# Optimization experiments

Hardware: AMD Instinct MI355X
Metric: run time of the kernel (lower is better)

## Reference

```python
import jax, jax.numpy as jnp
import numpy as np

H = 512      # hidden_size
NH = 8       # num_attention_heads
HD = H // NH # attention_head_size
B, S = 2, 4096


def setup_inputs() -> dict:
    key = jax.random.key(0)
    ks = jax.random.split(key, 9)
    sc = 1.0 / np.sqrt(H)
    return {
        "hidden_states": jax.random.normal(ks[0], (B, S, H), dtype=jnp.float32),
        "Wq": jax.random.normal(ks[1], (H, H), dtype=jnp.float32) * sc,
        "bq": jnp.zeros((H,), dtype=jnp.float32),
        "Wk": jax.random.normal(ks[2], (H, H), dtype=jnp.float32) * sc,
        "bk": jnp.zeros((H,), dtype=jnp.float32),
        "Wv": jax.random.normal(ks[3], (H, H), dtype=jnp.float32) * sc,
        "bv": jnp.zeros((H,), dtype=jnp.float32),
        "Wo": jax.random.normal(ks[4], (H, H), dtype=jnp.float32) * sc,
        "bo": jnp.zeros((H,), dtype=jnp.float32),
    }


def reference(hidden_states, Wq, bq, Wk, bk, Wv, bv, Wo, bo):
    # QKV projections (nn.Linear: x @ W.T + b)
    def split_heads(x):  # [B,S,H] -> [B,NH,S,HD]
        return x.reshape(B, S, NH, HD).transpose(0, 2, 1, 3)

    q = split_heads(hidden_states @ Wq.T + bq)
    k = split_heads(hidden_states @ Wk.T + bk)
    v = split_heads(hidden_states @ Wv.T + bv)

    scores = jnp.einsum("bhqd,bhkd->bhqk", q, k) / np.sqrt(HD)
    probs = jax.nn.softmax(scores, axis=-1)  # dropout is identity in eval
    ctx = jnp.einsum("bhqk,bhkd->bhqd", probs, v)
    ctx = ctx.transpose(0, 2, 1, 3).reshape(B, S, H)
    return ctx @ Wo.T + bo
```

## Files before the change

kernel.cpp:

```cpp
#include <hip/hip_runtime.h>
#include <hip/hip_bf16.h>
#include <math.h>


typedef __bf16 bf16;
typedef __bf16 bf16x2v __attribute__((ext_vector_type(2)));
typedef __bf16 bf16x4 __attribute__((ext_vector_type(4)));
typedef __bf16 bf16x8 __attribute__((ext_vector_type(8)));
typedef float  f32x4  __attribute__((ext_vector_type(4)));
typedef unsigned int u32x4 __attribute__((ext_vector_type(4)));

#define MFMA16(a, b, c) __builtin_amdgcn_mfma_f32_16x16x32_bf16((a), (b), (c), 0, 0, 0)

__device__ __forceinline__ void gll16(const bf16* g, bf16* l) {
    __builtin_amdgcn_global_load_lds(
        (const __attribute__((address_space(1))) void*)g,
        (__attribute__((address_space(3))) void*)l, 16, 0, 0);
}

__device__ __forceinline__ unsigned int pack2(float lo, float hi) {
    bf16x2v t = {(bf16)lo, (bf16)hi};
    return __builtin_bit_cast(unsigned int, t);
}

__global__ __launch_bounds__(256) void cvt_f32_bf16(const float* __restrict__ src,
                                                    bf16* __restrict__ dst, int n) {
    int i = (blockIdx.x * 256 + threadIdx.x) * 4;
    if (i >= n) return;
    float4 v = *reinterpret_cast<const float4*>(src + i);
    bf16x4 o = {(bf16)v.x, (bf16)v.y, (bf16)v.z, (bf16)v.w};
    *reinterpret_cast<bf16x4*>(dst + i) = o;
}

__global__ __launch_bounds__(256) void cvt_w4(const float* __restrict__ a,
                                              const float* __restrict__ b,
                                              const float* __restrict__ c,
                                              const float* __restrict__ d,
                                              bf16* __restrict__ out) {
    const int y = blockIdx.y;
    const float* src = (y == 0) ? a : (y == 1) ? b : (y == 2) ? c : d;
    int i = (blockIdx.x * 256 + threadIdx.x) * 4;
    float4 v = *reinterpret_cast<const float4*>(src + i);
    bf16x4 o = {(bf16)v.x, (bf16)v.y, (bf16)v.z, (bf16)v.w};
    *reinterpret_cast<bf16x4*>(out + y * 262144 + i) = o;
}

template <int MODE>
__global__ __launch_bounds__(256) void gemm_bt(const bf16* __restrict__ A,
                                               const bf16* __restrict__ W,
                                               const float* __restrict__ b0,
                                               const float* __restrict__ b1,
                                               const float* __restrict__ b2,
                                               bf16* __restrict__ dstbf,
                                               float* __restrict__ dstf) {
    __shared__ bf16 sA[128 * 64];
    __shared__ bf16 sB[128 * 64];

    const int tid = threadIdx.x;
    const int w   = tid >> 6;
    const int l   = tid & 63;
    const int m0  = blockIdx.y * 128;
    const int n0  = blockIdx.x * 128;
    const int z   = blockIdx.z;

    const bf16*  Wz   = (MODE == 0) ? (W + z * 262144) : W;
    const float* bias = (MODE == 0) ? (z == 0 ? b0 : (z == 1 ? b1 : b2)) : b0;
    const float  scale = (MODE == 0 && z == 0) ? 0.125f * 1.4426950408889634f : 1.0f;

    const int wr = (w >> 1) * 64, wc = (w & 1) * 64;
    const int fr = l & 15, fg = l >> 4;

    const int srow0 = tid >> 3;
    const int sgr   = (tid & 7) ^ (srow0 & 7);
    const int ldso  = srow0 * 64 + (tid & 7) * 8;

    f32x4 acc[4][4];
    const f32x4 zero = {0.f, 0.f, 0.f, 0.f};
#pragma unroll
    for (int i = 0; i < 4; i++)
#pragma unroll
        for (int j = 0; j < 4; j++) acc[i][j] = zero;

    for (int kt = 0; kt < 512; kt += 64) {
        __syncthreads();
#pragma unroll
        for (int p = 0; p < 4; p++) {
            const int row = srow0 + 32 * p;
            gll16(A  + (m0 + row) * 512 + kt + sgr * 8, &sA[p * 2048 + ldso]);
            gll16(Wz + (n0 + row) * 512 + kt + sgr * 8, &sB[p * 2048 + ldso]);
        }
        __syncthreads();

#pragma unroll
        for (int ks = 0; ks < 2; ks++) {
            bf16x8 af[4], bfg[4];
#pragma unroll
            for (int mi = 0; mi < 4; mi++)
                af[mi] = *reinterpret_cast<const bf16x8*>(
                    &sA[(wr + mi * 16 + fr) * 64 + (((4 * ks + fg) ^ (fr & 7)) << 3)]);
#pragma unroll
            for (int ni = 0; ni < 4; ni++)
                bfg[ni] = *reinterpret_cast<const bf16x8*>(
                    &sB[(wc + ni * 16 + fr) * 64 + (((4 * ks + fg) ^ (fr & 7)) << 3)]);
#pragma unroll
            for (int mi = 0; mi < 4; mi++)
#pragma unroll
                for (int ni = 0; ni < 4; ni++)
                    acc[mi][ni] = MFMA16(af[mi], bfg[ni], acc[mi][ni]);
        }
    }

#pragma unroll
    for (int mi = 0; mi < 4; mi++) {
#pragma unroll
        for (int ni = 0; ni < 4; ni++) {
            const int gcol = n0 + wc + ni * 16 + fr;
            const float bc = bias[gcol];
#pragma unroll
            for (int r = 0; r < 4; r++) {
                const int grow = m0 + wr + mi * 16 + fg * 4 + r;
                float v = acc[mi][ni][r] + bc;
                if (MODE == 0) {
                    v *= scale;
                    const int bb = grow >> 12, s = grow & 4095;
                    const int hh = gcol >> 6, dd = gcol & 63;
                    size_t idx;
                    if (z == 2) {
                        idx = (size_t)2 * 4194304 +
                              ((size_t)((bb * 8 + hh) * 64 + dd)) * 4096 + s;
                    } else {
                        idx = (size_t)z * 4194304 +
                              ((size_t)((bb * 8 + hh) * 4096 + s) << 6) + dd;
                    }
                    dstbf[idx] = (bf16)v;
                } else {
                    dstf[grow * 512 + gcol] = v;
                }
            }
        }
    }
}

__global__ __launch_bounds__(256, 2) void attn_kernel(const bf16* __restrict__ Q,
                                                      const bf16* __restrict__ K,
                                                      const bf16* __restrict__ Vt,
                                                      bf16* __restrict__ ctx) {
    __shared__ bf16 sKb[2][4096];
    __shared__ bf16 sVb[2][4096];

    const int tid = threadIdx.x;
    const int w   = tid >> 6;
    const int l   = tid & 63;
    const int fr  = l & 15, fg = l >> 4;

    int n = blockIdx.y * 32 + blockIdx.x;
    n = (n & 7) * 64 + (n >> 3);
    const int bh = n >> 5;
    const int q0 = (n & 31) * 128;
    const size_t base = (size_t)bh * 262144;

    const int srow0 = tid >> 3;
    const int sgr   = (tid & 7) ^ (srow0 & 7);
    const int ldso  = srow0 * 64 + (tid & 7) * 8;

    const int ko0 = fr * 64 + (((0 + fg) ^ (fr & 7)) << 3);
    const int ko1 = fr * 64 + (((4 + fg) ^ (fr & 7)) << 3);

#define STAGE(buf, tt)                                                              \
    do {                                                                            \
        _Pragma("unroll")                                                           \
        for (int p = 0; p < 2; p++) {                                               \
            const int row_ = srow0 + 32 * p;                                        \
            gll16(K  + base + (size_t)((tt) + row_) * 64 + sgr * 8,                 \
                  &sKb[buf][p * 2048 + ldso]);                                      \
            gll16(Vt + base + (size_t)row_ * 4096 + (tt) + sgr * 8,                 \
                  &sVb[buf][p * 2048 + ldso]);                                      \
        }                                                                           \
    } while (0)

    bf16x8 qf[2][2];
#pragma unroll
    for (int qb = 0; qb < 2; qb++)
#pragma unroll
        for (int ks = 0; ks < 2; ks++)
            qf[ks][qb] = *reinterpret_cast<const bf16x8*>(
                Q + base + (size_t)(q0 + 32 * w + 16 * qb + fr) * 64 + ks * 32 + fg * 8);

    const bf16 one = (bf16)1.0f;
    const bf16x8 ones = {one, one, one, one, one, one, one, one};

    const f32x4 zero = {0.f, 0.f, 0.f, 0.f};
    f32x4 o[4][2];
#pragma unroll
    for (int db = 0; db < 4; db++)
#pragma unroll
        for (int qb = 0; qb < 2; qb++) o[db][qb] = zero;
    f32x4 lacc[2] = {zero, zero};

    STAGE(0, 0);

    int pb = 0;
    for (int t = 0; t < 4096; t += 64, pb ^= 1) {
        __syncthreads();
        if (t + 64 < 4096) STAGE(pb ^ 1, t + 64);

        const bf16* kb = sKb[pb];
        const bf16* vb = sVb[pb];

        f32x4 sc[4][2];
        __builtin_amdgcn_s_setprio(1);
#pragma unroll
        for (int kvb = 0; kvb < 4; kvb++) {
            const bf16x8 kf0 = *reinterpret_cast<const bf16x8*>(kb + ko0 + kvb * 1024);
            const bf16x8 kf1 = *reinterpret_cast<const bf16x8*>(kb + ko1 + kvb * 1024);
#pragma unroll
            for (int qb = 0; qb < 2; qb++) {
                sc[kvb][qb] = MFMA16(kf0, qf[0][qb], zero);
                sc[kvb][qb] = MFMA16(kf1, qf[1][qb], sc[kvb][qb]);
            }
        }
        __builtin_amdgcn_s_setprio(0);

        bf16x8 vf[2][4];
#pragma unroll
        for (int db = 0; db < 4; db++) {
            vf[0][db] = *reinterpret_cast<const bf16x8*>(vb + ko0 + db * 1024);
            vf[1][db] = *reinterpret_cast<const bf16x8*>(vb + ko1 + db * 1024);
        }

        bf16x8 pf[2][2];
#pragma unroll
        for (int qb = 0; qb < 2; qb++) {
            unsigned int c[4][2];
#pragma unroll
            for (int kvb = 0; kvb < 4; kvb++) {
                const float p0 = __builtin_amdgcn_exp2f(sc[kvb][qb][0]);
                const float p1 = __builtin_amdgcn_exp2f(sc[kvb][qb][1]);
                const float p2 = __builtin_amdgcn_exp2f(sc[kvb][qb][2]);
                const float p3 = __builtin_amdgcn_exp2f(sc[kvb][qb][3]);
                c[kvb][0] = pack2(p0, p1);
                c[kvb][1] = pack2(p2, p3);
            }
#pragma unroll
            for (int ks = 0; ks < 2; ks++) {
                unsigned int a0 = c[2 * ks][0], b0 = c[2 * ks + 1][0];
                unsigned int a1 = c[2 * ks][1], b1 = c[2 * ks + 1][1];
                asm("v_permlane32_swap_b32 %0, %1" : "+v"(a0), "+v"(b0));
                asm("v_permlane16_swap_b32 %0, %1" : "+v"(a0), "+v"(b0));
                asm("v_permlane32_swap_b32 %0, %1" : "+v"(a1), "+v"(b1));
                asm("v_permlane16_swap_b32 %0, %1" : "+v"(a1), "+v"(b1));
                u32x4 uu = {a0, a1, b0, b1};
                pf[ks][qb] = __builtin_bit_cast(bf16x8, uu);
            }
        }

        __builtin_amdgcn_s_setprio(1);
#pragma unroll
        for (int ks = 0; ks < 2; ks++) {
#pragma unroll
            for (int qb = 0; qb < 2; qb++)
                lacc[qb] = MFMA16(ones, pf[ks][qb], lacc[qb]);
#pragma unroll
            for (int db = 0; db < 4; db++)
#pragma unroll
                for (int qb = 0; qb < 2; qb++)
                    o[db][qb] = MFMA16(vf[ks][db], pf[ks][qb], o[db][qb]);
        }
        __builtin_amdgcn_s_setprio(0);
    }

    const int bb = bh >> 3, hh = bh & 7;
#pragma unroll
    for (int qb = 0; qb < 2; qb++) {
        const float inv = 1.0f / lacc[qb][0];
        const int s = q0 + 32 * w + 16 * qb + fr;
#pragma unroll
        for (int db = 0; db < 4; db++) {
            bf16x4 pr = {(bf16)(o[db][qb][0] * inv), (bf16)(o[db][qb][1] * inv),
                         (bf16)(o[db][qb][2] * inv), (bf16)(o[db][qb][3] * inv)};
            *reinterpret_cast<bf16x4*>(
                &ctx[((size_t)(bb * 4096 + s)) * 512 + hh * 64 + db * 16 + 4 * fg]) = pr;
        }
    }
#undef STAGE
}

extern "C" void kernel_launch(void* const* d_in, const int* in_sizes, int n_in,
                              void* d_out, int out_size, void* d_ws, size_t ws_size,
                              hipStream_t stream) {
    const float* X  = (const float*)d_in[0];
    const float* Wq = (const float*)d_in[1];
    const float* bq = (const float*)d_in[2];
    const float* Wk = (const float*)d_in[3];
    const float* bk = (const float*)d_in[4];
    const float* Wv = (const float*)d_in[5];
    const float* bv = (const float*)d_in[6];
    const float* Wo = (const float*)d_in[7];
    const float* bo = (const float*)d_in[8];
    float* out = (float*)d_out;

    bf16* ws  = (bf16*)d_ws;
    bf16* Xbf = ws;
    bf16* Wqb = Xbf + 4194304;
    bf16* Qb  = Wqb + 4 * 262144;
    bf16* Kb  = Qb + 4194304;
    bf16* Vtb = Kb + 4194304;
    bf16* Ctx = Vtb + 4194304;

    cvt_f32_bf16<<<4096, 256, 0, stream>>>(X, Xbf, 4194304);
    cvt_w4<<<dim3(256, 4), 256, 0, stream>>>(Wq, Wk, Wv, Wo, Wqb);

    gemm_bt<0><<<dim3(4, 64, 3), 256, 0, stream>>>(Xbf, Wqb, bq, bk, bv, Qb, nullptr);

    attn_kernel<<<dim3(32, 16), 256, 0, stream>>>(Qb, Kb, Vtb, Ctx);

    gemm_bt<1><<<dim3(4, 64, 1), 256, 0, stream>>>(Ctx, Wqb + 3 * 262144, bo,
                                                   nullptr, nullptr, nullptr, out);
}
```

Baseline: 141.2 us.

## Software-pipeline attention loop: overlap QK of next tile with PV of previous

Restructures the flash-attention inner loop into a prologue/steady-state/epilogue pipeline. Each iteration now issues the QK MFMAs for tile t together with the PV MFMAs for tile t-1 in one high-priority block, then does the exp/pack and V reads for tile t. The goal is to interleave the transcendental softmax work with MFMA work and to cut the gaps between dependent phases. The cost is higher register pressure, because sc, pf and vf stay live across iterations.

```diff
diff --git a/kernel.cpp b/kernel.cpp
--- a/kernel.cpp
+++ b/kernel.cpp
@@ -178,6 +178,72 @@
         }                                                                           \
     } while (0)
 
+#define QK_TILE(kb_)                                                                \
+    do {                                                                            \
+        _Pragma("unroll")                                                           \
+        for (int kvb = 0; kvb < 4; kvb++) {                                         \
+            const bf16x8 kf0 = *reinterpret_cast<const bf16x8*>((kb_) + ko0 + kvb * 1024); \
+            const bf16x8 kf1 = *reinterpret_cast<const bf16x8*>((kb_) + ko1 + kvb * 1024); \
+            _Pragma("unroll")                                                       \
+            for (int qb = 0; qb < 2; qb++) {                                        \
+                sc[kvb][qb] = MFMA16(kf0, qf[0][qb], zero);                         \
+                sc[kvb][qb] = MFMA16(kf1, qf[1][qb], sc[kvb][qb]);                  \
+            }                                                                       \
+        }                                                                           \
+    } while (0)
+
+#define PV_TILE()                                                                   \
+    do {                                                                            \
+        _Pragma("unroll")                                                           \
+        for (int ks = 0; ks < 2; ks++) {                                            \
+            _Pragma("unroll")                                                       \
+            for (int qb = 0; qb < 2; qb++)                                          \
+                lacc[qb] = MFMA16(ones, pf[ks][qb], lacc[qb]);                      \
+            _Pragma("unroll")                                                       \
+            for (int db = 0; db < 4; db++)                                          \
+                _Pragma("unroll")                                                   \
+                for (int qb = 0; qb < 2; qb++)                                      \
+                    o[db][qb] = MFMA16(vf[ks][db], pf[ks][qb], o[db][qb]);          \
+        }                                                                           \
+    } while (0)
+
+#define VF_READ(vb_)                                                                \
+    do {                                                                            \
+        _Pragma("unroll")                                                           \
+        for (int db = 0; db < 4; db++) {                                            \
+            vf[0][db] = *reinterpret_cast<const bf16x8*>((vb_) + ko0 + db * 1024);  \
+            vf[1][db] = *reinterpret_cast<const bf16x8*>((vb_) + ko1 + db * 1024);  \
+        }                                                                           \
+    } while (0)
+
+#define SOFTMAX_PACK()                                                              \
+    do {                                                                            \
+        _Pragma("unroll")                                                           \
+        for (int qb = 0; qb < 2; qb++) {                                            \
+            unsigned int c[4][2];                                                   \
+            _Pragma("unroll")                                                       \
+            for (int kvb = 0; kvb < 4; kvb++) {                                     \
+                const float p0 = __builtin_amdgcn_exp2f(sc[kvb][qb][0]);            \
+                const float p1 = __builtin_amdgcn_exp2f(sc[kvb][qb][1]);            \
+                const float p2 = __builtin_amdgcn_exp2f(sc[kvb][qb][2]);            \
+                const float p3 = __builtin_amdgcn_exp2f(sc[kvb][qb][3]);            \
+                c[kvb][0] = pack2(p0, p1);                                          \
+                c[kvb][1] = pack2(p2, p3);                                          \
+            }                                                                       \
+            _Pragma("unroll")                                                       \
+            for (int ks = 0; ks < 2; ks++) {                                        \
+                unsigned int a0 = c[2 * ks][0], b0 = c[2 * ks + 1][0];              \
+                unsigned int a1 = c[2 * ks][1], b1 = c[2 * ks + 1][1];              \
+                asm("v_permlane32_swap_b32 %0, %1" : "+v"(a0), "+v"(b0));           \
+                asm("v_permlane16_swap_b32 %0, %1" : "+v"(a0), "+v"(b0));           \
+                asm("v_permlane32_swap_b32 %0, %1" : "+v"(a1), "+v"(b1));           \
+                asm("v_permlane16_swap_b32 %0, %1" : "+v"(a1), "+v"(b1));           \
+                u32x4 uu = {a0, a1, b0, b1};                                        \
+                pf[ks][qb] = __builtin_bit_cast(bf16x8, uu);                        \
+            }                                                                       \
+        }                                                                           \
+    } while (0)
+
     bf16x8 qf[2][2];
 #pragma unroll
     for (int qb = 0; qb < 2; qb++)
@@ -197,77 +263,34 @@
         for (int qb = 0; qb < 2; qb++) o[db][qb] = zero;
     f32x4 lacc[2] = {zero, zero};
 
+    f32x4  sc[4][2];
+    bf16x8 vf[2][4];
+    bf16x8 pf[2][2];
+
     STAGE(0, 0);
-
-    int pb = 0;
-    for (int t = 0; t < 4096; t += 64, pb ^= 1) {
+    __syncthreads();
+    STAGE(1, 64);
+    QK_TILE(sKb[0]);
+    VF_READ(sVb[0]);
+    SOFTMAX_PACK();
+
+    int pb = 1;
+    for (int t = 64; t < 4096; t += 64, pb ^= 1) {
         __syncthreads();
         if (t + 64 < 4096) STAGE(pb ^ 1, t + 64);
 
-        const bf16* kb = sKb[pb];
-        const bf16* vb = sVb[pb];
-
-        f32x4 sc[4][2];
         __builtin_amdgcn_s_setprio(1);
-#pragma unroll
-        for (int kvb = 0; kvb < 4; kvb++) {
-            const bf16x8 kf0 = *reinterpret_cast<const bf16x8*>(kb + ko0 + kvb * 1024);
-            const bf16x8 kf1 = *reinterpret_cast<const bf16x8*>(kb + ko1 + kvb * 1024);
-#pragma unroll
-            for (int qb = 0; qb < 2; qb++) {
-                sc[kvb][qb] = MFMA16(kf0, qf[0][qb], zero);
-                sc[kvb][qb] = MFMA16(kf1, qf[1][qb], sc[kvb][qb]);
-            }
-        }
+        QK_TILE(sKb[pb]);
+        PV_TILE();
         __builtin_amdgcn_s_setprio(0);
 
-        bf16x8 vf[2][4];
-#pragma unroll
-        for (int db = 0; db < 4; db++) {
-            vf[0][db] = *reinterpret_cast<const bf16x8*>(vb + ko0 + db * 1024);
-            vf[1][db] = *reinterpret_cast<const bf16x8*>(vb + ko1 + db * 1024);
-        }
-
-        bf16x8 pf[2][2];
-#pragma unroll
-        for (int qb = 0; qb < 2; qb++) {
-            unsigned int c[4][2];
-#pragma unroll
-            for (int kvb = 0; kvb < 4; kvb++) {
-                const float p0 = __builtin_amdgcn_exp2f(sc[kvb][qb][0]);
-                const float p1 = __builtin_amdgcn_exp2f(sc[kvb][qb][1]);
-                const float p2 = __builtin_amdgcn_exp2f(sc[kvb][qb][2]);
-                const float p3 = __builtin_amdgcn_exp2f(sc[kvb][qb][3]);
-                c[kvb][0] = pack2(p0, p1);
-                c[kvb][1] = pack2(p2, p3);
-            }
-#pragma unroll
-            for (int ks = 0; ks < 2; ks++) {
-                unsigned int a0 = c[2 * ks][0], b0 = c[2 * ks + 1][0];
-                unsigned int a1 = c[2 * ks][1], b1 = c[2 * ks + 1][1];
-                asm("v_permlane32_swap_b32 %0, %1" : "+v"(a0), "+v"(b0));
-                asm("v_permlane16_swap_b32 %0, %1" : "+v"(a0), "+v"(b0));
-                asm("v_permlane32_swap_b32 %0, %1" : "+v"(a1), "+v"(b1));
-                asm("v_permlane16_swap_b32 %0, %1" : "+v"(a1), "+v"(b1));
-                u32x4 uu = {a0, a1, b0, b1};
-                pf[ks][qb] = __builtin_bit_cast(bf16x8, uu);
-            }
-        }
-
-        __builtin_amdgcn_s_setprio(1);
-#pragma unroll
-        for (int ks = 0; ks < 2; ks++) {
-#pragma unroll
-            for (int qb = 0; qb < 2; qb++)
-                lacc[qb] = MFMA16(ones, pf[ks][qb], lacc[qb]);
-#pragma unroll
-            for (int db = 0; db < 4; db++)
-#pragma unroll
-                for (int qb = 0; qb < 2; qb++)
-                    o[db][qb] = MFMA16(vf[ks][db], pf[ks][qb], o[db][qb]);
-        }
-        __builtin_amdgcn_s_setprio(0);
+        VF_READ(sVb[pb]);
+        SOFTMAX_PACK();
     }
+
+    __builtin_amdgcn_s_setprio(1);
+    PV_TILE();
+    __builtin_amdgcn_s_setprio(0);
 
     const int bb = bh >> 3, hh = bh & 7;
 #pragma unroll
@@ -283,6 +306,10 @@
         }
     }
 #undef STAGE
+#undef QK_TILE
+#undef PV_TILE
+#undef VF_READ
+#undef SOFTMAX_PACK
 }
 
 extern "C" void kernel_launch(void* const* d_in, const int* in_sizes, int n_in,
```

After: 139.6 us. Within noise of the previous version (-1.1%).
